# Optimization experiments

Hardware: AMD Instinct MI355X
Metric: run time of the kernel (lower is better)

The kernel has to match this reference:

```python
import jax, jax.numpy as jnp
import numpy as np

B, N, DIM, H = 8, 1024, 768, 12
D = DIM // H
SCALE = D ** -0.5
EPS = 1e-5


def setup_inputs() -> dict:
    key = jax.random.key(0)
    ks = jax.random.split(key, 6)
    s = 0.02
    return {
        "x": jax.random.normal(ks[0], (B, N, DIM), jnp.float32),
        "w_qv": jax.random.normal(ks[1], (2 * DIM, DIM), jnp.float32) * s,
        "ext_k": jax.random.normal(ks[2], (1, H, N, D), jnp.float32),
        "ext_bias": jax.random.normal(ks[3], (1, H, N, N), jnp.float32),
        "bn_gamma": jnp.ones((H,), jnp.float32),
        "bn_beta": jnp.zeros((H,), jnp.float32),
        "w_proj": jax.random.normal(ks[4], (DIM, DIM), jnp.float32) * s,
        "b_proj": jnp.zeros((DIM,), jnp.float32),
    }


def reference(x, w_qv, ext_k, ext_bias, bn_gamma, bn_beta, w_proj, b_proj):
    b, n, c = x.shape
    # qv projection (no bias), split into q and v
    qv = jnp.einsum('bnc,ec->bne', x, w_qv)  # [B,N,2C]
    q, v = jnp.split(qv, 2, axis=-1)
    # b n (h d) -> b h n d
    q = q.reshape(b, n, H, D).transpose(0, 2, 1, 3)
    v = v.reshape(b, n, H, D).transpose(0, 2, 1, 3)
    # scores: (q @ ext_k^T + bias) * scale  -> [B,H,N,N]
    attn = (jnp.einsum('bhnd,xhmd->bhnm', q, ext_k) + ext_bias) * SCALE
    # BatchNorm2d over heads (training-mode batch stats over B,N,N)
    mean = jnp.mean(attn, axis=(0, 2, 3), keepdims=True)
    var = jnp.mean(jnp.square(attn - mean), axis=(0, 2, 3), keepdims=True)
    attn = (attn - mean) * jax.lax.rsqrt(var + EPS)
    attn = attn * bn_gamma[None, :, None, None] + bn_beta[None, :, None, None]
    # softmax over keys, dropout p=0
    attn = jax.nn.softmax(attn, axis=-1)
    out = jnp.einsum('bhnm,bhmd->bhnd', attn, v)
    out = out.transpose(0, 2, 1, 3).reshape(b, n, c)  # b h n d -> b n (h d)
    return jnp.einsum('bnc,oc->bno', out, w_proj) + b_proj
```

## Files before the change

kernel.cpp:

```cpp
#include <hip/hip_runtime.h>
#include <cstdint>

#define B_    8
#define N_    1024
#define DIM_  768
#define H_    12
#define D_    64
#define SCALE_ 0.125f
#define GQ_   32
#define GK_   4

typedef unsigned short u16;
typedef short bf16x8 __attribute__((ext_vector_type(8)));
typedef float f32x4  __attribute__((ext_vector_type(4)));

__device__ __forceinline__ u16 f2b(float f) {
  union { float f; unsigned u; } v; v.f = f;
  unsigned r = v.u + 0x7FFFu + ((v.u >> 16) & 1u);
  return (u16)(r >> 16);
}
__device__ __forceinline__ u16 phu(float f) {
  union { float f; unsigned u; } v; v.f = f;
  return (u16)((v.u + 0x8000u) >> 16);
}
__device__ __forceinline__ float b2f(u16 h) {
  union { unsigned u; float f; } v; v.u = ((unsigned)h) << 16; return v.f;
}
#if __has_builtin(__builtin_amdgcn_exp2f)
__device__ __forceinline__ float exp2fast(float x) { return __builtin_amdgcn_exp2f(x); }
#else
__device__ __forceinline__ float exp2fast(float x) { return __expf(x * 0.69314718f); }
#endif
__device__ __forceinline__ void gl2lds16(const void* g, void* l) {
  __builtin_amdgcn_global_load_lds(
      (const __attribute__((address_space(1))) void*)g,
      (__attribute__((address_space(3))) void*)l, 16, 0, 0);
}

__global__ __launch_bounds__(256) void cast_all(
    const float4* __restrict__ s0, u16* __restrict__ d0, int n0,
    const float4* __restrict__ s1, u16* __restrict__ d1, int n1,
    const float4* __restrict__ s2, u16* __restrict__ d2, int n2,
    const float4* __restrict__ s3, u16* __restrict__ d3, int n3,
    u16* __restrict__ ktT, float* __restrict__ zptr, int zfloats)
{
  const int tid = threadIdx.x;
  if (blockIdx.x == 0)
    for (int j = tid; j < zfloats; j += 256) zptr[j] = 0.f;
  int i = blockIdx.x * 256 + tid;
  const float4* s; u16* d; int off; int br;
  if (i < n0)               { s = s0; d = d0; off = i; br = 0; }
  else if (i < n0+n1)       { s = s1; d = d1; off = i - n0; br = 1; }
  else if (i < n0+n1+n2)    { s = s2; d = d2; off = i - n0 - n1; br = 2; }
  else if (i < n0+n1+n2+n3) { s = s3; d = d3; off = i - n0 - n1 - n2; br = 3; }
  else return;
  float4 v = s[off];
  ushort4 o; o.x = f2b(v.x); o.y = f2b(v.y); o.z = f2b(v.z); o.w = f2b(v.w);
  *(ushort4*)(d + (size_t)off * 4) = o;
  if (br == 3) {
    int flat = off * 4;
    int h = flat >> 16, rem = flat & 65535, n = rem >> 6, d4 = rem & 63;
    u16* kb = ktT + (h << 16) + (d4 << 10) + n;
    kb[0] = o.x; kb[1024] = o.y; kb[2048] = o.z; kb[3072] = o.w;
  }
}

__global__ __launch_bounds__(256) void qv_gemm(
    const u16* __restrict__ A, const u16* __restrict__ W,
    u16* __restrict__ qo, u16* __restrict__ vto)
{
  __shared__ u16 As[128*32];
  __shared__ u16 Bs[128*32];
  const int tid = threadIdx.x, lane = tid & 63, wid = tid >> 6;
  const int m0 = blockIdx.y * 128, n0 = blockIdx.x * 128;
  const int wm = (wid >> 1) * 64, wn = (wid & 1) * 64;
  const int lr = lane & 15, lq = lane >> 4;
  f32x4 acc[4][4] = {};
  for (int k0 = 0; k0 < 768; k0 += 32) {
#pragma unroll
    for (int it = 0; it < 2; ++it) {
      int c = it * 256 + tid;
      int row = c >> 2, c8 = c & 3;
      gl2lds16(A + (size_t)(m0 + row) * 768 + k0 + c8 * 8, (char*)As + (it*256 + wid*64) * 16);
      gl2lds16(W + (size_t)(n0 + row) * 768 + k0 + c8 * 8, (char*)Bs + (it*256 + wid*64) * 16);
    }
    __syncthreads();
    bf16x8 af[4], bfr[4];
#pragma unroll
    for (int i = 0; i < 4; ++i) {
      af[i]  = *(const bf16x8*)&As[(wm + i*16 + lr) * 32 + lq * 8];
      bfr[i] = *(const bf16x8*)&Bs[(wn + i*16 + lr) * 32 + lq * 8];
    }
#pragma unroll
    for (int mi = 0; mi < 4; ++mi)
#pragma unroll
      for (int nj = 0; nj < 4; ++nj)
        acc[mi][nj] = __builtin_amdgcn_mfma_f32_16x16x32_bf16(af[mi], bfr[nj], acc[mi][nj], 0, 0, 0);
    __syncthreads();
  }
  if (n0 < 768) {
#pragma unroll
    for (int mi = 0; mi < 4; ++mi)
#pragma unroll
      for (int nj = 0; nj < 4; ++nj)
#pragma unroll
        for (int r = 0; r < 4; ++r) {
          int row = m0 + wm + mi*16 + lq*4 + r;
          int col = n0 + wn + nj*16 + lr;
          int b = row >> 10, n = row & 1023;
          int h = col >> 6, d = col & 63;
          qo[(((size_t)(b*12 + h)) << 16) + (n << 6) + d] = f2b(acc[mi][nj][r]);
        }
  } else {
#pragma unroll
    for (int mi = 0; mi < 4; ++mi)
#pragma unroll
      for (int nj = 0; nj < 4; ++nj) {
        int rowb = m0 + wm + mi*16 + lq*4;
        int b = rowb >> 10, n = rowb & 1023;
        int e = n0 + wn + nj*16 + lr - 768;
        int h = e >> 6, d = e & 63;
        ushort4 o;
        o.x = f2b(acc[mi][nj][0]); o.y = f2b(acc[mi][nj][1]);
        o.z = f2b(acc[mi][nj][2]); o.w = f2b(acc[mi][nj][3]);
        *(ushort4*)(vto + (((size_t)(b*12 + h)) << 16) + (d << 10) + n) = o;
      }
  }
}

__global__ __launch_bounds__(256) void stats_fused(
    const u16* __restrict__ q, const u16* __restrict__ k,
    float* __restrict__ qs, float* __restrict__ qsum, float* __restrict__ ksum,
    float* __restrict__ Kgp, float* __restrict__ Qgp)
{
  __shared__ float t[64*68];
  const int h = blockIdx.y, bx = blockIdx.x, tid = threadIdx.x;
  if (bx < 64) {
    const int nl = tid >> 4, d4 = (tid & 15) * 4;
    const int n = bx * 16 + nl;
    float4 s = {0.f, 0.f, 0.f, 0.f};
#pragma unroll
    for (int b = 0; b < 8; ++b) {
      ushort4 u = *(const ushort4*)(q + (((size_t)(b*12 + h)) << 16) + (n << 6) + d4);
      s.x += b2f(u.x); s.y += b2f(u.y); s.z += b2f(u.z); s.w += b2f(u.w);
    }
    *(float4*)(qs + (((size_t)h) << 16) + (n << 6) + d4) = s;
    *(float4*)&t[nl*68 + d4] = s;
    __syncthreads();
    if (tid < 64) {
      float a = 0.f;
#pragma unroll
      for (int i = 0; i < 16; ++i) a += t[i*68 + tid];
      atomicAdd(&qsum[h*64 + tid], a);
    }
  } else if (bx == 100) {
    const int nl = tid >> 4, d4 = (tid & 15) * 4;
    float4 s = {0.f, 0.f, 0.f, 0.f};
    for (int n = nl; n < 1024; n += 16) {
      ushort4 u = *(const ushort4*)(k + (((size_t)h) << 16) + (n << 6) + d4);
      s.x += b2f(u.x); s.y += b2f(u.y); s.z += b2f(u.z); s.w += b2f(u.w);
    }
    *(float4*)&t[nl*68 + d4] = s;
    __syncthreads();
    if (tid < 64) {
      float a = 0.f;
#pragma unroll
      for (int i = 0; i < 16; ++i) a += t[i*68 + tid];
      ksum[h*64 + tid] = a;
    }
  } else {
    const int isQ = (bx >= 68);
    const int gx = isQ ? (bx - 68) : (bx - 64);
    const int r0 = gx * 256;
    const int rr = (tid >> 4) * 4, cc = (tid & 15) * 4;
    const u16* src = isQ ? q : k;
    float a[4][4] = {{0.f}};
    for (int t0 = 0; t0 < 256; t0 += 64) {
#pragma unroll
      for (int i = 0; i < 4; ++i) {
        int e = i*256 + tid; int r = e >> 4, d4 = (e & 15) * 4;
        int gr = r0 + t0 + r;
        size_t addr;
        if (isQ) { int b = gr >> 10, n = gr & 1023;
          addr = (((size_t)(b*12 + h)) << 16) + (n << 6) + d4; }
        else addr = (((size_t)h) << 16) + ((size_t)gr << 6) + d4;
        ushort4 u = *(const ushort4*)(src + addr);
        float4 f; f.x = b2f(u.x); f.y = b2f(u.y); f.z = b2f(u.z); f.w = b2f(u.w);
        *(float4*)&t[r*68 + d4] = f;
      }
      __syncthreads();
#pragma unroll 4
      for (int m = 0; m < 64; ++m) {
        float4 rv = *(const float4*)&t[m*68 + rr];
        float4 cv = *(const float4*)&t[m*68 + cc];
        a[0][0] += rv.x*cv.x; a[0][1] += rv.x*cv.y; a[0][2] += rv.x*cv.z; a[0][3] += rv.x*cv.w;
        a[1][0] += rv.y*cv.x; a[1][1] += rv.y*cv.y; a[1][2] += rv.y*cv.z; a[1][3] += rv.y*cv.w;
        a[2][0] += rv.z*cv.x; a[2][1] += rv.z*cv.y; a[2][2] += rv.z*cv.z; a[2][3] += rv.z*cv.w;
        a[3][0] += rv.w*cv.x; a[3][1] += rv.w*cv.y; a[3][2] += rv.w*cv.z; a[3][3] += rv.w*cv.w;
      }
      __syncthreads();
    }
    float* g = (isQ ? Qgp : Kgp) + (((size_t)gx) * 12 + h) * 4096;
#pragma unroll
    for (int i = 0; i < 4; ++i)
      *(float4*)&g[(rr + i)*64 + cc] = make_float4(a[i][0], a[i][1], a[i][2], a[i][3]);
  }
}

__global__ __launch_bounds__(256) void bias_stats(
    const float* __restrict__ bias, const u16* __restrict__ ktT,
    const float* __restrict__ qs, float* __restrict__ acc)
{
  __shared__ float red[12];
  const int tid = threadIdx.x, lane = tid & 63, wid = tid >> 6;
  const int lr = lane & 15, lq = lane >> 4;
  const int h = blockIdx.y;
  const int nb = blockIdx.x & 15, mb = blockIdx.x >> 4;
  const int n0 = nb * 64 + wid * 16;
  const size_t brow = (((size_t)h) << 20) + ((size_t)(n0 + lr) << 10);
  const size_t kbase = ((size_t)h) << 16;
  f32x4 kb[4] = {};
  float sb = 0.f, sb2 = 0.f;
#pragma unroll
  for (int ms = 0; ms < 4; ++ms) {
    const int m0 = mb * 256 + ms * 64;
#pragma unroll
    for (int ks = 0; ks < 2; ++ks) {
      const int mc = m0 + ks * 32 + lq * 8;
      float4 b0 = *(const float4*)(bias + brow + mc);
      float4 b1 = *(const float4*)(bias + brow + mc + 4);
      sb  += b0.x + b0.y + b0.z + b0.w + b1.x + b1.y + b1.z + b1.w;
      sb2 += b0.x*b0.x + b0.y*b0.y + b0.z*b0.z + b0.w*b0.w
           + b1.x*b1.x + b1.y*b1.y + b1.z*b1.z + b1.w*b1.w;
      union { bf16x8 v; u16 u[8]; } af;
      af.u[0] = f2b(b0.x); af.u[1] = f2b(b0.y); af.u[2] = f2b(b0.z); af.u[3] = f2b(b0.w);
      af.u[4] = f2b(b1.x); af.u[5] = f2b(b1.y); af.u[6] = f2b(b1.z); af.u[7] = f2b(b1.w);
#pragma unroll
      for (int dj = 0; dj < 4; ++dj) {
        bf16x8 bfr = *(const bf16x8*)(ktT + kbase + (size_t)(dj*16 + lr) * 1024 + mc);
        kb[dj] = __builtin_amdgcn_mfma_f32_16x16x32_bf16(af.v, bfr, kb[dj], 0, 0, 0);
      }
    }
  }
  float cross = 0.f;
#pragma unroll
  for (int dj = 0; dj < 4; ++dj)
#pragma unroll
    for (int r = 0; r < 4; ++r)
      cross += kb[dj][r] *
               qs[kbase + ((size_t)(nb*64 + wid*16 + lq*4 + r) << 6) + dj*16 + lr];
#pragma unroll
  for (int s = 32; s; s >>= 1) {
    sb += __shfl_xor(sb, s); sb2 += __shfl_xor(sb2, s); cross += __shfl_xor(cross, s);
  }
  if (lane == 0) { red[wid] = sb; red[4 + wid] = sb2; red[8 + wid] = cross; }
  __syncthreads();
  if (tid == 0) {
    atomicAdd(acc + h,      red[0] + red[1] + red[2] + red[3]);
    atomicAdd(acc + 12 + h, red[4] + red[5] + red[6] + red[7]);
    atomicAdd(acc + 24 + h, red[8] + red[9] + red[10] + red[11]);
  }
}

__global__ __launch_bounds__(256) void finalize_kernel(
    const float* __restrict__ qsum, const float* __restrict__ ksum,
    const float* __restrict__ Qgp, const float* __restrict__ Kgp,
    const float* __restrict__ acc, const float* __restrict__ gamma,
    float* __restrict__ temp)
{
  __shared__ float qg[4096];
  __shared__ float kg[4096];
  __shared__ float red[8];
  int h = blockIdx.x, tid = threadIdx.x, wid = tid >> 6, lane = tid & 63;
#pragma unroll
  for (int i = 0; i < 16; ++i) {
    int e = i*256 + tid;
    float q = 0.f, k = 0.f;
    for (int g = 0; g < GQ_; ++g) q += Qgp[(((size_t)g)*12 + h)*4096 + e];
#pragma unroll
    for (int g = 0; g < GK_; ++g) k += Kgp[(((size_t)g)*12 + h)*4096 + e];
    qg[e] = q; kg[e] = k;
  }
  __syncthreads();
  float s2 = 0.f;
#pragma unroll
  for (int i = 0; i < 16; ++i) { int e = i*256 + tid; s2 += qg[e]*kg[e]; }
  float s1 = (tid < 64) ? qsum[h*64 + tid] * ksum[h*64 + tid] : 0.f;
#pragma unroll
  for (int s = 32; s; s >>= 1) { s2 += __shfl_xor(s2, s); s1 += __shfl_xor(s1, s); }
  if (lane == 0) { red[wid] = s2; red[4 + wid] = s1; }
  __syncthreads();
  if (tid == 0) {
    double S2 = (double)red[0] + red[1] + red[2] + red[3];
    double S1 = (double)red[4];
    double M = 8388608.0;
    double Sb = acc[h], Sb2 = acc[12 + h], Cross = acc[24 + h];
    double Eraw  = (S1 + 8.0 * Sb) / M;
    double Eraw2 = (S2 + 2.0 * Cross + 8.0 * Sb2) / M;
    double var = (double)SCALE_ * (double)SCALE_ * (Eraw2 - Eraw * Eraw);
    double rstd = 1.0 / sqrt(var + 1e-5);
    temp[h] = (float)((double)gamma[h] * (double)SCALE_ * rstd);
  }
}

__global__ __launch_bounds__(256) void attn_kernel(
    const u16* __restrict__ q, const u16* __restrict__ k, const u16* __restrict__ vT,
    const float* __restrict__ bias, const float* __restrict__ temp, u16* __restrict__ out)
{
  __shared__ u16 kt[4096];
  __shared__ u16 vt[5120];
  __shared__ u16 pt[128*72];
  const int tid = threadIdx.x, lane = tid & 63, wid = tid >> 6;
  const int lr = lane & 15, lq = lane >> 4;
  const int X = blockIdx.x;
  const int g = X >> 6, r_ = X & 63, b = r_ >> 3, q8 = r_ & 7;
  const int p = g*8 + q8;
  const int h = p % 12, n0 = (p / 12) * 128;
  const size_t qbase = ((((size_t)b) * 12 + h) << 16) + ((size_t)n0 << 6);
  const size_t kbase = ((size_t)h) << 16;
  const size_t vbase = ((((size_t)b) * 12 + h) << 16);
  const size_t bbase = (((size_t)h) << 20) + ((size_t)n0 << 10);
  const float tmp2 = temp[h] * 1.44269504f;
  const int W = wid * 32;

  bf16x8 aq[2][2];
#pragma unroll
  for (int mi = 0; mi < 2; ++mi)
#pragma unroll
    for (int ks = 0; ks < 2; ++ks)
      aq[mi][ks] = *(const bf16x8*)(q + qbase + (size_t)(W + mi*16 + lr)*64 + ks*32 + lq*8);

  for (int i = tid; i < 1024; i += 256) {
    int ks = i >> 9, rr = (i >> 5) & 15, cc = i & 31;
    vt[ks*2560 + (64 + rr)*32 + cc] = (rr == 0) ? (u16)0x3F80 : (u16)0;
  }

  const float* br[2][4];
#pragma unroll
  for (int mi = 0; mi < 2; ++mi)
#pragma unroll
    for (int r = 0; r < 4; ++r)
      br[mi][r] = bias + bbase + (size_t)(W + mi*16 + lq*4 + r) * 1024 + lr;

  f32x4 oacc[5][2] = {};

  for (int m0 = 0; m0 < 1024; m0 += 64) {
#pragma unroll
    for (int it = 0; it < 2; ++it) {
      int c = it*256 + tid; int ks = c >> 8, r = (c >> 2) & 63, c8 = c & 3;
      gl2lds16(k  + kbase + (size_t)(m0 + r) * 64 + ks*32 + c8*8, (char*)kt + (it*256 + wid*64) * 16);
      gl2lds16(vT + vbase + (size_t)r * 1024 + m0 + ks*32 + c8*8, (char*)vt + it*5120 + wid*1024);
    }
    f32x4 s[2][4];
#pragma unroll
    for (int mi = 0; mi < 2; ++mi)
#pragma unroll
      for (int nj = 0; nj < 4; ++nj)
#pragma unroll
        for (int r = 0; r < 4; ++r)
          s[mi][nj][r] = br[mi][r][m0 + nj*16];
    __syncthreads();
#pragma unroll
    for (int ks = 0; ks < 2; ++ks) {
#pragma unroll
      for (int nj = 0; nj < 4; ++nj) {
        bf16x8 bk = *(const bf16x8*)&kt[ks*2048 + (nj*16 + lr)*32 + lq*8];
#pragma unroll
        for (int mi = 0; mi < 2; ++mi)
          s[mi][nj] = __builtin_amdgcn_mfma_f32_16x16x32_bf16(aq[mi][ks], bk, s[mi][nj], 0, 0, 0);
      }
    }
#pragma unroll
    for (int mi = 0; mi < 2; ++mi)
#pragma unroll
      for (int r = 0; r < 4; ++r) {
        int row = W + mi*16 + lq*4 + r;
#pragma unroll
        for (int nj = 0; nj < 4; ++nj)
          pt[row*72 + nj*16 + lr] = phu(exp2fast(s[mi][nj][r] * tmp2));
      }
#pragma unroll
    for (int ks = 0; ks < 2; ++ks) {
      bf16x8 bp[2];
#pragma unroll
      for (int ni = 0; ni < 2; ++ni)
        bp[ni] = *(const bf16x8*)&pt[(W + ni*16 + lr)*72 + ks*32 + lq*8];
#pragma unroll
      for (int dj = 0; dj < 5; ++dj) {
        bf16x8 av = *(const bf16x8*)&vt[ks*2560 + (dj*16 + lr)*32 + lq*8];
#pragma unroll
        for (int ni = 0; ni < 2; ++ni)
          oacc[dj][ni] = __builtin_amdgcn_mfma_f32_16x16x32_bf16(av, bp[ni], oacc[dj][ni], 0, 0, 0);
      }
    }
    __syncthreads();
  }
#pragma unroll
  for (int ni = 0; ni < 2; ++ni) {
    float l = __shfl(oacc[4][ni][0], lr);
    float linv = __builtin_amdgcn_rcpf(l);
    int n = n0 + W + ni*16 + lr;
    u16* orow = out + (size_t)(b*1024 + n) * 768 + h*64 + lq*4;
#pragma unroll
    for (int dj = 0; dj < 4; ++dj) {
      ushort4 o;
      o.x = f2b(oacc[dj][ni][0] * linv); o.y = f2b(oacc[dj][ni][1] * linv);
      o.z = f2b(oacc[dj][ni][2] * linv); o.w = f2b(oacc[dj][ni][3] * linv);
      *(ushort4*)(orow + dj*16) = o;
    }
  }
}

__global__ __launch_bounds__(256) void proj_gemm(
    const u16* __restrict__ A, const u16* __restrict__ W,
    const float* __restrict__ bp, float* __restrict__ out)
{
  __shared__ u16 As[128*32];
  __shared__ u16 Bs[128*32];
  const int tid = threadIdx.x, lane = tid & 63, wid = tid >> 6;
  const int m0 = blockIdx.y * 128, n0 = blockIdx.x * 128;
  const int wm = (wid >> 1) * 64, wn = (wid & 1) * 64;
  const int lr = lane & 15, lq = lane >> 4;
  f32x4 acc[4][4] = {};
  for (int k0 = 0; k0 < 768; k0 += 32) {
#pragma unroll
    for (int it = 0; it < 2; ++it) {
      int c = it*256 + tid; int row = c >> 2, c8 = c & 3;
      gl2lds16(A + (size_t)(m0 + row) * 768 + k0 + c8*8, (char*)As + (it*256 + wid*64) * 16);
      gl2lds16(W + (size_t)(n0 + row) * 768 + k0 + c8*8, (char*)Bs + (it*256 + wid*64) * 16);
    }
    __syncthreads();
    bf16x8 af[4], bfr[4];
#pragma unroll
    for (int i = 0; i < 4; ++i) {
      af[i]  = *(const bf16x8*)&As[(wm + i*16 + lr)*32 + lq*8];
      bfr[i] = *(const bf16x8*)&Bs[(wn + i*16 + lr)*32 + lq*8];
    }
#pragma unroll
    for (int mi = 0; mi < 4; ++mi)
#pragma unroll
      for (int nj = 0; nj < 4; ++nj)
        acc[mi][nj] = __builtin_amdgcn_mfma_f32_16x16x32_bf16(af[mi], bfr[nj], acc[mi][nj], 0, 0, 0);
    __syncthreads();
  }
#pragma unroll
  for (int mi = 0; mi < 4; ++mi)
#pragma unroll
    for (int nj = 0; nj < 4; ++nj)
#pragma unroll
      for (int r = 0; r < 4; ++r) {
        int row = m0 + wm + mi*16 + lq*4 + r;
        int col = n0 + wn + nj*16 + lr;
        out[(size_t)row * 768 + col] = acc[mi][nj][r] + bp[col];
      }
}

extern "C" void kernel_launch(void* const* d_in, const int* in_sizes, int n_in,
                              void* d_out, int out_size, void* d_ws, size_t ws_size,
                              hipStream_t stream)
{
  const float* x     = (const float*)d_in[0];
  const float* wqv   = (const float*)d_in[1];
  const float* ek    = (const float*)d_in[2];
  const float* ebias = (const float*)d_in[3];
  const float* gamma = (const float*)d_in[4];
  const float* wp    = (const float*)d_in[6];
  const float* bp    = (const float*)d_in[7];
  float* out = (float*)d_out;

  char* ws = (char*)d_ws;
  size_t off = 0;
  auto alloc = [&](size_t bytes) { char* p = ws + off; off += (bytes + 255) & ~(size_t)255; return p; };
  u16* x16   = (u16*)alloc((size_t)8192*768*2);
  u16* wqv16 = (u16*)alloc((size_t)1536*768*2);
  u16* wp16  = (u16*)alloc((size_t)768*768*2);
  u16* k16   = (u16*)alloc((size_t)12*1024*64*2);
  u16* ktT16 = (u16*)alloc((size_t)12*64*1024*2);
  u16* q16   = (u16*)alloc((size_t)8*12*1024*64*2);
  u16* vt16  = (u16*)alloc((size_t)8*12*1024*64*2);
  float* qs  = (float*)alloc((size_t)12*1024*64*4);
  float* acc = (float*)alloc(3*12*4);
  float* qsum = (float*)alloc(12*64*4);
  float* ksum = (float*)alloc(12*64*4);
  int zfloats = (int)(((size_t)(((char*)ksum + 12*64*4) - (char*)acc)) / 4);
  float* temp = (float*)alloc(12*4);
  float* Qgp = (float*)x16;
  float* Kgp = Qgp + (size_t)GQ_*12*4096;
  u16* attn16 = x16;

  {
    int c0 = 8192*768/4, c1 = 1536*768/4, c2 = 768*768/4, c3 = 12*1024*64/4;
    int total = c0 + c1 + c2 + c3;
    cast_all<<<(total + 255)/256, 256, 0, stream>>>(
        (const float4*)x, x16, c0, (const float4*)wqv, wqv16, c1,
        (const float4*)wp, wp16, c2, (const float4*)ek, k16, c3,
        ktT16, acc, zfloats);
  }
  qv_gemm<<<dim3(12, 64), 256, 0, stream>>>(x16, wqv16, q16, vt16);
  stats_fused<<<dim3(101, 12), 256, 0, stream>>>(q16, k16, qs, qsum, ksum, Kgp, Qgp);
  bias_stats<<<dim3(64, 12), 256, 0, stream>>>(ebias, ktT16, qs, acc);
  finalize_kernel<<<12, 256, 0, stream>>>(qsum, ksum, Qgp, Kgp, acc, gamma, temp);
  attn_kernel<<<dim3(768), 256, 0, stream>>>(q16, k16, vt16, ebias, temp, attn16);
  proj_gemm<<<dim3(6, 64), 256, 0, stream>>>(attn16, wp16, bp, out);
}
```

Baseline: 295.4 us.

## Pre-cast ext_bias to swizzled bf16 layout for stats and attention

The cast kernel now also converts the 48 MB fp32 ext_bias into a bf16 copy whose columns are permuted within each 64-wide block. This lets attn_kernel fetch one ushort4 per row instead of four strided scalar floats, and lets bias_stats load bf16x8 directly. ktT's column layout is swizzled to match, so the MFMA reduction in bias_stats stays consistent. The aim is to halve bias traffic in the attention kernel, which reads it once per batch (8 times). The cost is an extra pass that reads the fp32 bias and scatters 2-byte writes, plus bias precision cut to bf16, which also affects the batch-norm statistics.

```diff
diff --git a/kernel.cpp b/kernel.cpp
--- a/kernel.cpp
+++ b/kernel.cpp
@@ -42,25 +42,42 @@
     const float4* __restrict__ s1, u16* __restrict__ d1, int n1,
     const float4* __restrict__ s2, u16* __restrict__ d2, int n2,
     const float4* __restrict__ s3, u16* __restrict__ d3, int n3,
+    const float4* __restrict__ sb, u16* __restrict__ bias_sw, int nb,
     u16* __restrict__ ktT, float* __restrict__ zptr, int zfloats)
 {
   const int tid = threadIdx.x;
   if (blockIdx.x == 0)
     for (int j = tid; j < zfloats; j += 256) zptr[j] = 0.f;
   int i = blockIdx.x * 256 + tid;
+  int tot = n0 + n1 + n2 + n3;
+  if (i >= tot) {
+    int ib = i - tot;
+    if (ib >= nb) return;
+    float4 v = sb[ib];
+    int flat = ib * 4;
+    int h = flat >> 20, rem = flat & 1048575;
+    int n = rem >> 10, g0 = rem & 1023;
+    int base = g0 & ~63, w = g0 & 63;
+    u16* dst = bias_sw + ((size_t)h << 20) + ((size_t)n << 10) + base;
+    dst[((w+0) & 15)*4 + ((w+0) >> 4)] = f2b(v.x);
+    dst[((w+1) & 15)*4 + ((w+1) >> 4)] = f2b(v.y);
+    dst[((w+2) & 15)*4 + ((w+2) >> 4)] = f2b(v.z);
+    dst[((w+3) & 15)*4 + ((w+3) >> 4)] = f2b(v.w);
+    return;
+  }
   const float4* s; u16* d; int off; int br;
   if (i < n0)               { s = s0; d = d0; off = i; br = 0; }
   else if (i < n0+n1)       { s = s1; d = d1; off = i - n0; br = 1; }
   else if (i < n0+n1+n2)    { s = s2; d = d2; off = i - n0 - n1; br = 2; }
-  else if (i < n0+n1+n2+n3) { s = s3; d = d3; off = i - n0 - n1 - n2; br = 3; }
-  else return;
+  else                      { s = s3; d = d3; off = i - n0 - n1 - n2; br = 3; }
   float4 v = s[off];
   ushort4 o; o.x = f2b(v.x); o.y = f2b(v.y); o.z = f2b(v.z); o.w = f2b(v.w);
   *(ushort4*)(d + (size_t)off * 4) = o;
   if (br == 3) {
     int flat = off * 4;
-    int h = flat >> 16, rem = flat & 65535, n = rem >> 6, d4 = rem & 63;
-    u16* kb = ktT + (h << 16) + (d4 << 10) + n;
+    int h = flat >> 16, rem = flat & 65535, m = rem >> 6, d4 = rem & 63;
+    int msw = (m & ~63) + ((m & 15) << 2) + ((m & 63) >> 4);
+    u16* kb = ktT + (h << 16) + (d4 << 10) + msw;
     kb[0] = o.x; kb[1024] = o.y; kb[2048] = o.z; kb[3072] = o.w;
   }
 }
@@ -208,7 +225,7 @@
 }
 
 __global__ __launch_bounds__(256) void bias_stats(
-    const float* __restrict__ bias, const u16* __restrict__ ktT,
+    const u16* __restrict__ bias_sw, const u16* __restrict__ ktT,
     const float* __restrict__ qs, float* __restrict__ acc)
 {
   __shared__ float red[12];
@@ -217,8 +234,8 @@
   const int h = blockIdx.y;
   const int nb = blockIdx.x & 15, mb = blockIdx.x >> 4;
   const int n0 = nb * 64 + wid * 16;
-  const size_t brow = (((size_t)h) << 20) + ((size_t)(n0 + lr) << 10);
-  const size_t kbase = ((size_t)h) << 16;
+  const size_t brow = ((size_t)h << 20) + ((size_t)(n0 + lr) << 10);
+  const size_t kbase = (size_t)h << 16;
   f32x4 kb[4] = {};
   float sb = 0.f, sb2 = 0.f;
 #pragma unroll
@@ -227,14 +244,10 @@
 #pragma unroll
     for (int ks = 0; ks < 2; ++ks) {
       const int mc = m0 + ks * 32 + lq * 8;
-      float4 b0 = *(const float4*)(bias + brow + mc);
-      float4 b1 = *(const float4*)(bias + brow + mc + 4);
-      sb  += b0.x + b0.y + b0.z + b0.w + b1.x + b1.y + b1.z + b1.w;
-      sb2 += b0.x*b0.x + b0.y*b0.y + b0.z*b0.z + b0.w*b0.w
-           + b1.x*b1.x + b1.y*b1.y + b1.z*b1.z + b1.w*b1.w;
       union { bf16x8 v; u16 u[8]; } af;
-      af.u[0] = f2b(b0.x); af.u[1] = f2b(b0.y); af.u[2] = f2b(b0.z); af.u[3] = f2b(b0.w);
-      af.u[4] = f2b(b1.x); af.u[5] = f2b(b1.y); af.u[6] = f2b(b1.z); af.u[7] = f2b(b1.w);
+      af.v = *(const bf16x8*)(bias_sw + brow + mc);
+#pragma unroll
+      for (int j = 0; j < 8; ++j) { float x = b2f(af.u[j]); sb += x; sb2 += x*x; }
 #pragma unroll
       for (int dj = 0; dj < 4; ++dj) {
         bf16x8 bfr = *(const bf16x8*)(ktT + kbase + (size_t)(dj*16 + lr) * 1024 + mc);
@@ -305,7 +318,7 @@
 
 __global__ __launch_bounds__(256) void attn_kernel(
     const u16* __restrict__ q, const u16* __restrict__ k, const u16* __restrict__ vT,
-    const float* __restrict__ bias, const float* __restrict__ temp, u16* __restrict__ out)
+    const u16* __restrict__ bias_sw, const float* __restrict__ temp, u16* __restrict__ out)
 {
   __shared__ u16 kt[4096];
   __shared__ u16 vt[5120];
@@ -335,12 +348,12 @@
     vt[ks*2560 + (64 + rr)*32 + cc] = (rr == 0) ? (u16)0x3F80 : (u16)0;
   }
 
-  const float* br[2][4];
+  const u16* br16[2][4];
 #pragma unroll
   for (int mi = 0; mi < 2; ++mi)
 #pragma unroll
     for (int r = 0; r < 4; ++r)
-      br[mi][r] = bias + bbase + (size_t)(W + mi*16 + lq*4 + r) * 1024 + lr;
+      br16[mi][r] = bias_sw + bbase + (size_t)(W + mi*16 + lq*4 + r) * 1024 + lr*4;
 
   f32x4 oacc[5][2] = {};
 
@@ -355,10 +368,11 @@
 #pragma unroll
     for (int mi = 0; mi < 2; ++mi)
 #pragma unroll
-      for (int nj = 0; nj < 4; ++nj)
-#pragma unroll
-        for (int r = 0; r < 4; ++r)
-          s[mi][nj][r] = br[mi][r][m0 + nj*16];
+      for (int r = 0; r < 4; ++r) {
+        ushort4 u = *(const ushort4*)(br16[mi][r] + m0);
+        s[mi][0][r] = b2f(u.x); s[mi][1][r] = b2f(u.y);
+        s[mi][2][r] = b2f(u.z); s[mi][3][r] = b2f(u.w);
+      }
     __syncthreads();
 #pragma unroll
     for (int ks = 0; ks < 2; ++ks) {
@@ -478,6 +492,7 @@
   u16* ktT16 = (u16*)alloc((size_t)12*64*1024*2);
   u16* q16   = (u16*)alloc((size_t)8*12*1024*64*2);
   u16* vt16  = (u16*)alloc((size_t)8*12*1024*64*2);
+  u16* bsw16 = (u16*)alloc((size_t)12*1024*1024*2);
   float* qs  = (float*)alloc((size_t)12*1024*64*4);
   float* acc = (float*)alloc(3*12*4);
   float* qsum = (float*)alloc(12*64*4);
@@ -490,16 +505,17 @@
 
   {
     int c0 = 8192*768/4, c1 = 1536*768/4, c2 = 768*768/4, c3 = 12*1024*64/4;
-    int total = c0 + c1 + c2 + c3;
+    int cb = 12*1024*1024/4;
+    int total = c0 + c1 + c2 + c3 + cb;
     cast_all<<<(total + 255)/256, 256, 0, stream>>>(
         (const float4*)x, x16, c0, (const float4*)wqv, wqv16, c1,
         (const float4*)wp, wp16, c2, (const float4*)ek, k16, c3,
-        ktT16, acc, zfloats);
+        (const float4*)ebias, bsw16, cb, ktT16, acc, zfloats);
   }
   qv_gemm<<<dim3(12, 64), 256, 0, stream>>>(x16, wqv16, q16, vt16);
   stats_fused<<<dim3(101, 12), 256, 0, stream>>>(q16, k16, qs, qsum, ksum, Kgp, Qgp);
-  bias_stats<<<dim3(64, 12), 256, 0, stream>>>(ebias, ktT16, qs, acc);
+  bias_stats<<<dim3(64, 12), 256, 0, stream>>>(bsw16, ktT16, qs, acc);
   finalize_kernel<<<12, 256, 0, stream>>>(qsum, ksum, Qgp, Kgp, acc, gamma, temp);
-  attn_kernel<<<dim3(768), 256, 0, stream>>>(q16, k16, vt16, ebias, temp, attn16);
+  attn_kernel<<<dim3(768), 256, 0, stream>>>(q16, k16, vt16, bsw16, temp, attn16);
   proj_gemm<<<dim3(6, 64), 256, 0, stream>>>(attn16, wp16, bp, out);
 }
```

New measurement: 315.2 us. 1.07x slower.
